# Performance work log

Hardware: AMD Instinct MI355X
Metric: run time of the kernel (lower is better)

Reference implementation:

```python
import jax, jax.numpy as jnp
import numpy as np


def _lstm_bi(x, wih, whh, b):
    # x: [B,T,D]; wih: [2,D,4H]; whh: [2,H,4H]; b: [2,4H]. PyTorch gate order i,f,g,o.
    def run(xs, wi, wh, bb):
        B, H = xs.shape[1], wh.shape[0]
        def step(carry, xt):
            h, c = carry
            g = xt @ wi + h @ wh + bb
            i, f, gg, o = jnp.split(g, 4, axis=-1)
            c = jax.nn.sigmoid(f) * c + jax.nn.sigmoid(i) * jnp.tanh(gg)
            h = jax.nn.sigmoid(o) * jnp.tanh(c)
            return (h, c), h
        z0 = jnp.zeros((B, H), xs.dtype)
        _, hs = jax.lax.scan(step, (z0, z0), xs)
        return hs
    xs = jnp.swapaxes(x, 0, 1)  # [T,B,D]
    hf = run(xs, wih[0], whh[0], b[0])
    hb = run(xs[::-1], wih[1], whh[1], b[1])[::-1]
    return jnp.swapaxes(jnp.concatenate([hf, hb], axis=-1), 0, 1)


def _norm_thr(att, thr):
    # sum-normalize, threshold-sparsify, renormalize (PSP core)
    att = att / (jnp.sum(att, -1, keepdims=True) + 1e-8)
    att = jnp.where(att > thr, att, jnp.zeros_like(att))
    return att / (jnp.sum(att, -1, keepdims=True) + 1e-8)


def _ln(x, g, b):
    mu = jnp.mean(x, -1, keepdims=True)
    var = jnp.mean(jnp.square(x - mu), -1, keepdims=True)
    return (x - mu) / jnp.sqrt(var + 1e-6) * g + b


def _forward(audio, video, thr_val, fa_w1, fa_w2, av_aw, av_ab, av_vw, av_vb,
             av_v2w, av_gw, av_hw, fv_w1, fv_w2, la_wih, la_whh, la_b,
             lv_wih, lv_whh, lv_b, vL1, vL2, aL1, aL2, vfc, afc, ln_g, ln_b, L1w, L2w):
    bs, T = audio.shape[0], audio.shape[1]
    fa = (audio @ fa_w1) @ fa_w2                          # [B,T,128]
    vf = video.reshape(bs, T, -1, video.shape[-1])        # [B,T,49,512]
    # AVGA audio-guided visual attention
    v_h = jax.nn.relu(vf @ av_vw + av_vb)                 # [B,T,49,512]
    a_h = jax.nn.relu(fa @ av_aw + av_ab)                 # [B,T,512]
    content = v_h @ av_v2w + (a_h @ av_gw)[..., None]     # [B,T,49,49]
    z = jnp.squeeze(jnp.tanh(content) @ av_hw, -1)        # [B,T,49]
    alpha = jax.nn.softmax(z, -1)
    video_t = jnp.einsum('btp,btpd->btd', alpha, vf)      # [B,T,512]
    video_t = (video_t @ fv_w1) @ fv_w2                   # [B,T,128]
    # bidirectional LSTMs
    lstm_a = _lstm_bi(fa, la_wih, la_whh, la_b)           # [B,T,256]
    lstm_v = _lstm_bi(video_t, lv_wih, lv_whh, lv_b)      # [B,T,256]
    # PSP (eval mode: dropout is identity)
    v_b1 = jax.nn.relu(lstm_v @ vL1)
    v_b2 = jax.nn.relu(lstm_v @ vL2)
    a_b1 = jax.nn.relu(lstm_a @ aL1)
    a_b2 = jax.nn.relu(lstm_a @ aL2)
    scale = 1.0 / jnp.sqrt(jnp.asarray(v_b2.shape[-1], v_b2.dtype))
    att = jax.nn.relu(jnp.einsum('bvd,bad->bva', v_b2, a_b1) * scale)  # v->a raw
    att_v2a = _norm_thr(att, thr_val)
    att_a2v = _norm_thr(jnp.swapaxes(att, 1, 2), thr_val)
    v_psp = lstm_v + jnp.einsum('bva,bad->bvd', att_v2a, a_b2)
    a_psp = lstm_a + jnp.einsum('bav,bvd->bad', att_a2v, v_b1)
    v_psp = _ln(jax.nn.relu(v_psp @ vfc), ln_g, ln_b)
    a_psp = _ln(jax.nn.relu(a_psp @ afc), ln_g, ln_b)
    fuse = 0.5 * (v_psp + a_psp)
    vn = v_psp / jnp.maximum(jnp.linalg.norm(v_psp, axis=-1, keepdims=True), 1e-12)
    an = a_psp / jnp.maximum(jnp.linalg.norm(a_psp, axis=-1, keepdims=True), 1e-12)
    cross_att = jnp.sum(vn * an, -1)                      # [B,T]
    out = jax.nn.relu(fuse @ L1w) @ L2w                   # [B,T,29]
    return (fuse, out, cross_att)


def setup_inputs() -> dict:
    key = jax.random.key(0)
    ks = iter(jax.random.split(key, 40))
    def w(*shape):
        fan_in = shape[-2] if len(shape) > 1 else shape[-1]
        return jax.random.normal(next(ks), shape, jnp.float32) * (1.0 / np.sqrt(fan_in))
    B, T = 256, 10
    return dict(
        audio=jax.random.normal(next(ks), (B, T, 128), jnp.float32),
        video=jax.random.normal(next(ks), (B, T, 7, 7, 512), jnp.float32),
        thr_val=jnp.float32(0.099),
        fa_w1=w(128, 256), fa_w2=w(256, 128),
        av_aw=w(128, 512), av_ab=jnp.zeros((512,), jnp.float32),
        av_vw=w(512, 512), av_vb=jnp.zeros((512,), jnp.float32),
        av_v2w=w(512, 49), av_gw=w(512, 49), av_hw=w(49, 1),
        fv_w1=w(512, 256), fv_w2=w(256, 128),
        la_wih=w(2, 128, 512), la_whh=w(2, 128, 512), la_b=jnp.zeros((2, 512), jnp.float32),
        lv_wih=w(2, 128, 512), lv_whh=w(2, 128, 512), lv_b=jnp.zeros((2, 512), jnp.float32),
        vL1=w(256, 256), vL2=w(256, 256), aL1=w(256, 256), aL2=w(256, 256),
        vfc=w(256, 256), afc=w(256, 256),
        ln_g=jnp.ones((256,), jnp.float32), ln_b=jnp.zeros((256,), jnp.float32),
        L1w=w(256, 64), L2w=w(64, 29),
    )


def reference(audio, video, thr_val, fa_w1, fa_w2, av_aw, av_ab, av_vw, av_vb,
              av_v2w, av_gw, av_hw, fv_w1, fv_w2, la_wih, la_whh, la_b,
              lv_wih, lv_whh, lv_b, vL1, vL2, aL1, aL2, vfc, afc, ln_g, ln_b, L1w, L2w):
    return _forward(audio, video, thr_val, fa_w1, fa_w2, av_aw, av_ab, av_vw, av_vb,
                    av_v2w, av_gw, av_hw, fv_w1, fv_w2, la_wih, la_whh, la_b,
                    lv_wih, lv_whh, lv_b, vL1, vL2, aL1, aL2, vfc, afc, ln_g, ln_b, L1w, L2w)
```

## Files before the change

### kernel.cpp

```cpp
#include <hip/hip_runtime.h>
#include <math.h>

#define DEV __device__ __forceinline__

typedef _Float16 f16x8 __attribute__((ext_vector_type(8)));
typedef _Float16 f16x4 __attribute__((ext_vector_type(4)));
typedef float    f32x4 __attribute__((ext_vector_type(4)));

typedef __attribute__((address_space(1))) const void gvoid_t;
typedef __attribute__((address_space(3))) void lvoid_t;

DEV void gload_lds16(const char* g, char* l){
    __builtin_amdgcn_global_load_lds((gvoid_t*)g, (lvoid_t*)l, 16, 0, 0);
}

DEV float sigmoidf_(float x){ return 1.0f/(1.0f + expf(-x)); }

DEV float wred64(float x){
    #pragma unroll
    for (int off=32; off; off>>=1) x += __shfl_xor(x, off);
    return x;
}

#define MFMA16(a,b,c) __builtin_amdgcn_mfma_f32_16x16x32_f16(a,b,c,0,0,0)

DEV void packone(const float* __restrict__ src, int N, int NfrTot, int nfOff,
                 _Float16* __restrict__ Dh, _Float16* __restrict__ Dl, int o){
    int j = o&7, l16 = (o>>3)&15, kg = (o>>7)&3;
    int rest = o>>9;
    int nfl = rest % (N>>4), kt = rest / (N>>4);
    int k = kt*32 + kg*8 + j, n = nfl*16 + l16;
    float x = src[(size_t)k*N + n];
    _Float16 h = (_Float16)x;
    size_t d = ((size_t)kt*NfrTot + nfOff + nfl)*512 + kg*128 + l16*8 + j;
    Dh[d] = h; Dl[d] = (_Float16)(x - (float)h);
}

__global__ __launch_bounds__(256) void k_prep(
    const float* __restrict__ fa_w1, const float* __restrict__ fa_w2, float* __restrict__ faW,
    const float* __restrict__ fv_w1, const float* __restrict__ fv_w2,
    const float* __restrict__ av_vw, _Float16* __restrict__ Bh, _Float16* __restrict__ Bl,
    const float* __restrict__ v2w, _Float16* __restrict__ Wh, _Float16* __restrict__ Wl,
    const float* __restrict__ lv_wih,
    _Float16* __restrict__ PKfv_h, _Float16* __restrict__ PKfv_l,
    _Float16* __restrict__ PKxv_h, _Float16* __restrict__ PKxv_l)
{
    int bid = blockIdx.x, t = threadIdx.x;
    if (bid < 64){
        int idx = bid*256+t; int m = idx>>7, n = idx&127;
        float acc=0.f;
        for (int k=0;k<256;k++) acc += fa_w1[m*256+k]*fa_w2[k*128+n];
        faW[idx]=acc;
    } else if (bid < 1088){
        int o = (bid-64)*256+t;
        int j = o & 7, l16 = (o>>3)&15, kg = (o>>7)&3, nf = (o>>9)&31, kt = o>>14;
        int k = kt*32 + kg*8 + j, n = nf*16 + l16;
        float x = av_vw[(size_t)k*512 + n];
        _Float16 h = (_Float16)x;
        Bh[o] = h; Bl[o] = (_Float16)(x - (float)h);
    } else if (bid < 1216){
        int o = (bid-1088)*256+t;
        int j = o & 7, l16 = (o>>3)&15, kg = (o>>7)&3, qf = (o>>9)&3, kbg = o>>11;
        int k = kbg*32 + kg*8 + j, q = qf*16 + l16;
        float x = (q < 49) ? v2w[(size_t)k*49 + q] : 0.f;
        _Float16 h = (_Float16)x;
        Wh[o] = h; Wl[o] = (_Float16)(x - (float)h);
    } else if (bid < 1472){
        int o = (bid-1216)*256+t;
        int j=o&7, l16=(o>>3)&15, kg=(o>>7)&3; int rest=o>>9;
        int nfl = rest&7, kt = rest>>3;
        int k = kt*32+kg*8+j, n = nfl*16+l16;
        float acc=0.f;
        for (int kk=0;kk<256;kk++) acc += fv_w1[k*256+kk]*fv_w2[kk*128+n];
        _Float16 h=(_Float16)acc;
        size_t d = ((size_t)kt*8 + nfl)*512 + kg*128 + l16*8 + j;
        PKfv_h[d]=h; PKfv_l[d]=(_Float16)(acc-(float)h);
    } else {
        int seg = (bid-1472)>>8;
        int o = ((bid-1472)&255)*256+t;
        packone(lv_wih + (size_t)seg*65536, 512, 64, seg*32, PKxv_h, PKxv_l, o);
    }
}

__global__ __launch_bounds__(256) void k_faga2(
    const float* __restrict__ audio, const float* __restrict__ faW,
    const float* __restrict__ av_aw, const float* __restrict__ av_ab,
    const float* __restrict__ av_gw,
    const float* __restrict__ la_wih, const float* __restrict__ la_b,
    float* __restrict__ gGA, float* __restrict__ xpA)
{
    int b0 = blockIdx.x*8; int t = threadIdx.x;
    __shared__ float sau[8][128], sfa[8][128], sah[8][512];
    for (int i=t;i<1024;i+=256){ int bt=i>>7,k=i&127; sau[bt][k]=audio[(size_t)(b0+bt)*128+k]; }
    __syncthreads();
    for (int u=0;u<4;u++){
        int i=t+u*256, bt=i>>7, n=i&127;
        float acc=0.f;
        for (int k4=0;k4<32;k4++){
            float4 x4=*(const float4*)&sau[bt][k4*4];
            acc+=x4.x*faW[(k4*4)*128+n]+x4.y*faW[(k4*4+1)*128+n]
                +x4.z*faW[(k4*4+2)*128+n]+x4.w*faW[(k4*4+3)*128+n];
        }
        sfa[bt][n]=acc;
    }
    __syncthreads();
    for (int u=0;u<2;u++){
        int n=t+u*256;
        float bv=av_ab[n];
        float acc[8]={bv,bv,bv,bv,bv,bv,bv,bv};
        for (int k4=0;k4<32;k4++){
            float w0=av_aw[(k4*4)*512+n], w1=av_aw[(k4*4+1)*512+n],
                  w2=av_aw[(k4*4+2)*512+n], w3=av_aw[(k4*4+3)*512+n];
            #pragma unroll
            for (int bt=0;bt<8;bt++){
                float4 x4=*(const float4*)&sfa[bt][k4*4];
                acc[bt]+=x4.x*w0+x4.y*w1+x4.z*w2+x4.w*w3;
            }
        }
        #pragma unroll
        for (int bt=0;bt<8;bt++) sah[bt][n]=fmaxf(acc[bt],0.f);
    }
    __syncthreads();
    for (int hh=0;hh<2;hh++){
        if (t<196){
            int bt=hh*4 + t/49, q=t%49;
            float acc=0.f;
            for (int k=0;k<512;k++) acc+=sah[bt][k]*av_gw[k*49+q];
            gGA[(size_t)(b0+bt)*49+q]=acc;
        }
    }
    for (int u=0;u<4;u++){
        int n = t + u*256;
        int dir = n >> 9, g = n & 511;
        const float* W = la_wih + (size_t)dir*65536;
        float bvv = la_b[dir*512 + g];
        float acc[8] = {bvv,bvv,bvv,bvv,bvv,bvv,bvv,bvv};
        for (int k4=0;k4<32;k4++){
            float w0=W[(k4*4+0)*512+g], w1=W[(k4*4+1)*512+g],
                  w2=W[(k4*4+2)*512+g], w3=W[(k4*4+3)*512+g];
            #pragma unroll
            for (int bt=0;bt<8;bt++){
                float4 x4=*(const float4*)&sfa[bt][k4*4];
                acc[bt]+=x4.x*w0+x4.y*w1+x4.z*w2+x4.w*w3;
            }
        }
        #pragma unroll
        for (int bt=0;bt<8;bt++)
            xpA[((size_t)(b0+bt))*1024 + n] = acc[bt];
    }
}

DEV void cvt4_(float4 v, f16x4& hv, f16x4& lv){
    hv[0]=(_Float16)v.x; lv[0]=(_Float16)(v.x-(float)hv[0]);
    hv[1]=(_Float16)v.y; lv[1]=(_Float16)(v.y-(float)hv[1]);
    hv[2]=(_Float16)v.z; lv[2]=(_Float16)(v.z-(float)hv[2]);
    hv[3]=(_Float16)v.w; lv[3]=(_Float16)(v.w-(float)hv[3]);
}

__global__ __launch_bounds__(256,2) void k_avga_fused(
    const float* __restrict__ video,
    const _Float16* __restrict__ Bh, const _Float16* __restrict__ Bl,
    const float* __restrict__ bias,
    const _Float16* __restrict__ Wh, const _Float16* __restrict__ Wl,
    const float* __restrict__ gGA, const float* __restrict__ hw,
    float* __restrict__ vT)
{
    __shared__ __align__(16) char smem[81920];
    int bt = blockIdx.x;
    int t = threadIdx.x;
    int lane = t & 63, w = t >> 6;
    int l16 = lane & 15, lq = lane >> 4;
    int lb = lane * 16;
    int w8 = w*8192;
    const char* BhB = (const char*)Bh;

    int am = t >> 3, ak = (t & 7) * 4;
    int aoff1 = ((am>>4)*4 + (ak>>3))*256 + (am&15)*16 + (ak&7)*2;
    int am2 = am + 32;
    int aoff2 = ((am2>>4)*4 + (ak>>3))*256 + (am2&15)*16 + (ak&7)*2;
    size_t r1 = (size_t)bt*49 + am;  if (r1 > 125439) r1 = 125439;
    size_t r2 = (size_t)bt*49 + am2; if (r2 > 125439) r2 = 125439;
    const float* Arow1 = video + r1*512 + ak;
    const float* Arow2 = video + r2*512 + ak;

    const f32x4 vzero = {0.f,0.f,0.f,0.f};
    f32x4 acc[4][8];
    #pragma unroll
    for (int p=0;p<4;p++)
        #pragma unroll
        for (int q=0;q<8;q++) acc[p][q] = vzero;

    float4 pa0, pa1;
    pa0 = *(const float4*)(Arow1);
    pa1 = *(const float4*)(Arow2);
    {
        f16x4 hv, lv;
        char* h = &smem[0];
        cvt4_(pa0, hv, lv);
        *(f16x4*)(h + aoff1) = hv; *(f16x4*)(h + 4096 + aoff1) = lv;
        cvt4_(pa1, hv, lv);
        *(f16x4*)(h + aoff2) = hv; *(f16x4*)(h + 4096 + aoff2) = lv;
        #pragma unroll
        for (int i=0;i<8;i++)
            gload_lds16(BhB + w8 + i*1024 + lane*16,
                        &smem[16384] + w8 + i*1024 + lane*16);
    }
    __syncthreads();

    for (int kt = 0; kt < 16; ++kt){
        int cur = kt & 1;
        bool more = (kt < 15);
        if (more){
            pa0 = *(const float4*)(Arow1 + (kt+1)*32);
            pa1 = *(const float4*)(Arow2 + (kt+1)*32);
            const char* srcb = BhB + (size_t)(kt+1)*32768 + w8;
            char* dstb = &smem[16384 + (cur^1)*32768] + w8;
            #pragma unroll
            for (int i=0;i<8;i++)
                gload_lds16(srcb + i*1024 + lane*16, dstb + i*1024 + lane*16);
        }
        const char* aB = &smem[cur*8192];
        f16x8 ah[4], al[4];
        #pragma unroll
        for (int p=0;p<4;p++){
            ah[p] = *(const f16x8*)(aB + p*1024 + lb);
            al[p] = *(const f16x8*)(aB + 4096 + p*1024 + lb);
        }
        const char* bB = &smem[16384 + cur*32768];
        #pragma unroll
        for (int q=0;q<8;q++){
            f16x8 bh  = *(const f16x8*)(bB + (w*8+q)*1024 + lb);
            f16x8 bl2 = *(const f16x8*)(Bl + (size_t)kt*16384 + (size_t)(w*8+q)*512 + lane*8);
            #pragma unroll
            for (int p=0;p<4;p++){
                acc[p][q] = MFMA16(ah[p], bh,  acc[p][q]);
                acc[p][q] = MFMA16(ah[p], bl2, acc[p][q]);
                acc[p][q] = MFMA16(al[p], bh,  acc[p][q]);
            }
        }
        if (more){
            char* h = &smem[(cur^1)*8192];
            f16x4 hv, lv;
            cvt4_(pa0, hv, lv);
            *(f16x4*)(h + aoff1) = hv; *(f16x4*)(h + 4096 + aoff1) = lv;
            cvt4_(pa1, hv, lv);
            *(f16x4*)(h + aoff2) = hv; *(f16x4*)(h + 4096 + aoff2) = lv;
        }
        __syncthreads();
    }

    float bv[8];
    #pragma unroll
    for (int q=0;q<8;q++) bv[q] = bias[w*128 + q*16 + l16];

    char* vh = &smem[16384 + w*8192];
    f32x4 cacc[4][4];
    #pragma unroll
    for (int p=0;p<4;p++)
        #pragma unroll
        for (int qf=0;qf<4;qf++) cacc[p][qf] = vzero;

    #pragma unroll
    for (int c=0;c<4;c++){
        #pragma unroll
        for (int p=0;p<4;p++)
            #pragma unroll
            for (int qq=0;qq<2;qq++){
                int q = c*2 + qq;
                int offbase = p*1024 + (qq*2 + (l16>>3))*256 + (l16&7)*2;
                #pragma unroll
                for (int r=0;r<4;r++){
                    float x = fmaxf(acc[p][q][r] + bv[q], 0.f);
                    _Float16 hh = (_Float16)x;
                    _Float16 ll = (_Float16)(x - (float)hh);
                    int off = offbase + (lq*4 + r)*16;
                    *(_Float16*)(vh + off)        = hh;
                    *(_Float16*)(vh + 4096 + off) = ll;
                }
            }
        int kbg = w*4 + c;
        f16x8 vhh[4], vhl[4];
        #pragma unroll
        for (int p=0;p<4;p++){
            vhh[p] = *(const f16x8*)(vh + p*1024 + lb);
            vhl[p] = *(const f16x8*)(vh + 4096 + p*1024 + lb);
        }
        #pragma unroll
        for (int qf=0;qf<4;qf++){
            size_t wo = (size_t)kbg*2048 + qf*512 + lane*8;
            f16x8 wh = *(const f16x8*)(Wh + wo);
            f16x8 wl = *(const f16x8*)(Wl + wo);
            #pragma unroll
            for (int p=0;p<4;p++){
                cacc[p][qf] = MFMA16(vhh[p], wh, cacc[p][qf]);
                cacc[p][qf] = MFMA16(vhh[p], wl, cacc[p][qf]);
                cacc[p][qf] = MFMA16(vhl[p], wh, cacc[p][qf]);
            }
        }
    }

    __syncthreads();
    float* pw = (float*)&smem[w*16384];
    #pragma unroll
    for (int p=0;p<4;p++)
        #pragma unroll
        for (int qf=0;qf<4;qf++)
            #pragma unroll
            for (int r=0;r<4;r++)
                pw[(p*16 + lq*4 + r)*64 + qf*16 + l16] = cacc[p][qf][r];
    __syncthreads();
    float* cb = (float*)&smem[0];
    for (int i=t; i<4096; i+=256)
        cb[i] = cb[i] + cb[4096+i] + cb[8192+i] + cb[12288+i];
    __syncthreads();

    float* szp    = (float*)&smem[65536];
    float* salpha = (float*)&smem[66560];
    if (t < 196){
        int p = t >> 2, ds = t & 3;
        float ga = gGA[(size_t)bt*49 + p];
        float part = 0.f;
        for (int q = ds*13; q < ds*13+13 && q < 49; q++)
            part += tanhf(cb[p*64 + q] + ga) * hw[q];
        szp[t] = part;
    }
    __syncthreads();
    if (t < 64){
        float z = (t<49) ? (szp[t*4]+szp[t*4+1]+szp[t*4+2]+szp[t*4+3]) : -1e30f;
        float m = z;
        #pragma unroll
        for (int off=32; off; off>>=1) m = fmaxf(m, __shfl_xor(m, off));
        float e = (t<49)? expf(z - m) : 0.f;
        float s = e;
        #pragma unroll
        for (int off=32; off; off>>=1) s += __shfl_xor(s, off);
        salpha[t] = e / s;
    }
    __syncthreads();
    const float* vb = video + (size_t)bt*49*512;
    #pragma unroll
    for (int u=0;u<2;u++){
        int d = t + u*256;
        float a0 = 0.f;
        for (int p=0;p<49;p++) a0 += salpha[p] * vb[(size_t)p*512 + d];
        vT[(size_t)bt*512 + d] = a0;
    }
}

template<int MP, int NQ, bool BIAS, bool RELU>
__global__ __launch_bounds__(256) void k_gemm(
    const float* __restrict__ A, int lda,
    const _Float16* __restrict__ Wh, const _Float16* __restrict__ Wl,
    const float* __restrict__ bias,
    float* __restrict__ C, int ldc,
    int nkt, int Nfr)
{
    __shared__ __align__(16) char sA[2][MP*2048];
    int t = threadIdx.x, lane = t&63, w = t>>6;
    int l16 = lane&15, lq = lane>>4, lb = lane*16;
    int row0 = blockIdx.x * (MP*16);
    int nf0 = blockIdx.y * (4*NQ) + w*NQ;

    int am = t>>3, ak = (t&7)*4;
    int aoff = ((am>>4)*4 + (ak>>3))*256 + (am&15)*16 + (ak&7)*2;
    const float* Arow = A + (size_t)(row0+am)*lda + ak;

    const f32x4 vzero = {0.f,0.f,0.f,0.f};
    f32x4 acc[MP][NQ];
    #pragma unroll
    for (int p=0;p<MP;p++)
        #pragma unroll
        for (int q=0;q<NQ;q++) acc[p][q] = vzero;

    float4 pa = *(const float4*)(Arow);
    {
        f16x4 hv, lv;
        char* h = &sA[0][0];
        cvt4_(pa, hv, lv);
        *(f16x4*)(h + aoff) = hv; *(f16x4*)(h + MP*1024 + aoff) = lv;
    }
    __syncthreads();

    for (int kt = 0; kt < nkt; ++kt){
        int cur = kt & 1;
        bool more = (kt+1 < nkt);
        if (more) pa = *(const float4*)(Arow + (kt+1)*32);
        const char* aB = &sA[cur][0];
        f16x8 ah[MP], al[MP];
        #pragma unroll
        for (int p=0;p<MP;p++){
            ah[p] = *(const f16x8*)(aB + p*1024 + lb);
            al[p] = *(const f16x8*)(aB + MP*1024 + p*1024 + lb);
        }
        #pragma unroll
        for (int q=0;q<NQ;q++){
            size_t bo = ((size_t)kt*Nfr + nf0 + q)*512 + lane*8;
            f16x8 bh  = *(const f16x8*)(Wh + bo);
            f16x8 bl2 = *(const f16x8*)(Wl + bo);
            #pragma unroll
            for (int p=0;p<MP;p++){
                acc[p][q] = MFMA16(ah[p], bh,  acc[p][q]);
                acc[p][q] = MFMA16(ah[p], bl2, acc[p][q]);
                acc[p][q] = MFMA16(al[p], bh,  acc[p][q]);
            }
        }
        if (more){
            char* h = &sA[cur^1][0];
            f16x4 hv, lv;
            cvt4_(pa, hv, lv);
            *(f16x4*)(h + aoff) = hv; *(f16x4*)(h + MP*1024 + aoff) = lv;
        }
        __syncthreads();
    }

    #pragma unroll
    for (int q=0;q<NQ;q++){
        int n = (nf0+q)*16 + l16;
        float bv = BIAS ? bias[n] : 0.f;
        #pragma unroll
        for (int p=0;p<MP;p++){
            #pragma unroll
            for (int r=0;r<4;r++){
                float v = acc[p][q][r] + bv;
                if (RELU) v = fmaxf(v, 0.f);
                C[(size_t)(row0 + p*16 + lq*4 + r)*ldc + n] = v;
            }
        }
    }
}

__global__ __launch_bounds__(256) void k_lstm(
    const float* __restrict__ xpA, const float* __restrict__ xpV,
    const float* __restrict__ la_whh, const float* __restrict__ lv_whh,
    float* __restrict__ lstm_a, float* __restrict__ lstm_v)
{
    int blk = blockIdx.x;
    int c = blk >> 6;
    int chunk = blk & 63;
    int t = threadIdx.x;
    int j  = t & 127;
    int bh = t >> 7;
    const float* whh = ((c<2)? la_whh : lv_whh) + (size_t)(c&1)*128*512;
    const float* xpm = (c<2)? xpA : xpV;
    float* outp = (c<2)? lstm_a : lstm_v;
    int dir = c & 1;

    __shared__ float hbuf[4][128];
    float cc[2] = {0.f,0.f};
    for (int i=t;i<512;i+=256) ((float*)hbuf)[i] = 0.f;
    __syncthreads();

    for (int s=0; s<10; s++){
        int tt = dir ? (9-s) : s;
        float gi[2], gf[2], gg[2], go[2];
        #pragma unroll
        for (int b=0;b<2;b++){
            int gb = chunk*4 + bh*2 + b;
            const float* xrow = xpm + ((size_t)gb*10 + tt)*1024 + dir*512;
            gi[b]=xrow[j]; gf[b]=xrow[128+j]; gg[b]=xrow[256+j]; go[b]=xrow[384+j];
        }
        #pragma unroll 4
        for (int k=0;k<128;k++){
            float wi = whh[k*512 + j];
            float wf = whh[k*512 + 128 + j];
            float wg = whh[k*512 + 256 + j];
            float wo = whh[k*512 + 384 + j];
            #pragma unroll
            for (int b=0;b<2;b++){
                float hk = hbuf[bh*2+b][k];
                gi[b] += hk*wi; gf[b] += hk*wf; gg[b] += hk*wg; go[b] += hk*wo;
            }
        }
        __syncthreads();
        #pragma unroll
        for (int b=0;b<2;b++){
            float i_ = sigmoidf_(gi[b]);
            float f_ = sigmoidf_(gf[b]);
            float g_ = tanhf(gg[b]);
            float o_ = sigmoidf_(go[b]);
            cc[b] = f_*cc[b] + i_*g_;
            float h_ = o_*tanhf(cc[b]);
            hbuf[bh*2+b][j] = h_;
            int gb = chunk*4 + bh*2 + b;
            outp[((size_t)gb*10 + tt)*256 + dir*128 + j] = h_;
        }
        __syncthreads();
    }
}

__global__ __launch_bounds__(256) void k_tail(
    const float* __restrict__ lstm_a, const float* __restrict__ lstm_v,
    const float* __restrict__ vL1, const float* __restrict__ vL2,
    const float* __restrict__ aL1, const float* __restrict__ aL2,
    const float* __restrict__ vfc, const float* __restrict__ afc,
    const float* __restrict__ thrp,
    const float* __restrict__ ln_g, const float* __restrict__ ln_b,
    const float* __restrict__ L1w, const float* __restrict__ L2w,
    float* __restrict__ dout)
{
    int b = blockIdx.x, t = threadIdx.x;
    int lane = t & 63, w = t >> 6;
    __shared__ float sla[10][256], slv[10][256];
    __shared__ float sb1v[10][256], sb2v[10][256], sb1a[10][256], sb2a[10][256];
    __shared__ float sfu[10][256];
    __shared__ float s64[10][64];
    __shared__ float satt[100], s_v2a[100], s_a2v[100];
    __shared__ float sredp[160];
    __shared__ float scos[120];

    size_t base = (size_t)b*2560;
    for (int i=t;i<2560;i+=256){
        ((float*)sla)[i] = lstm_a[base+i];
        ((float*)slv)[i] = lstm_v[base+i];
    }
    __syncthreads();

    {
        float a1[10], a2[10];
        #pragma unroll
        for (int r=0;r<10;r++){ a1[r]=0.f; a2[r]=0.f; }
        #pragma unroll 4
        for (int k=0;k<256;k++){
            float w1 = vL1[k*256+t], w2 = vL2[k*256+t];
            #pragma unroll
            for (int r=0;r<10;r++){ float x=slv[r][k]; a1[r]+=x*w1; a2[r]+=x*w2; }
        }
        #pragma unroll
        for (int r=0;r<10;r++){ sb1v[r][t]=fmaxf(a1[r],0.f); sb2v[r][t]=fmaxf(a2[r],0.f); }
        #pragma unroll
        for (int r=0;r<10;r++){ a1[r]=0.f; a2[r]=0.f; }
        #pragma unroll 4
        for (int k=0;k<256;k++){
            float w1 = aL1[k*256+t], w2 = aL2[k*256+t];
            #pragma unroll
            for (int r=0;r<10;r++){ float x=sla[r][k]; a1[r]+=x*w1; a2[r]+=x*w2; }
        }
        #pragma unroll
        for (int r=0;r<10;r++){ sb1a[r][t]=fmaxf(a1[r],0.f); sb2a[r][t]=fmaxf(a2[r],0.f); }
    }
    __syncthreads();

    if (t < 100){
        int v = t/10, a = t - v*10;
        float acc=0.f;
        for (int k=0;k<256;k++) acc += sb2v[v][k]*sb1a[a][k];
        satt[t] = fmaxf(acc*(1.0f/16.0f), 0.f);
    }
    __syncthreads();
    float thr = thrp[0];
    if (t < 10){
        int v = t;
        float rs=0.f; for(int a=0;a<10;a++) rs += satt[v*10+a];
        float inv = 1.f/(rs+1e-8f);
        float tmp[10]; float rs2=0.f;
        for(int a=0;a<10;a++){ float x = satt[v*10+a]*inv; x = (x>thr)?x:0.f; tmp[a]=x; rs2+=x; }
        float inv2 = 1.f/(rs2+1e-8f);
        for(int a=0;a<10;a++) s_v2a[v*10+a] = tmp[a]*inv2;
    } else if (t>=16 && t<26){
        int a = t-16;
        float cs=0.f; for(int v=0;v<10;v++) cs += satt[v*10+a];
        float inv = 1.f/(cs+1e-8f);
        float tmp[10]; float cs2=0.f;
        for(int v=0;v<10;v++){ float x = satt[v*10+a]*inv; x=(x>thr)?x:0.f; tmp[v]=x; cs2+=x; }
        float inv2 = 1.f/(cs2+1e-8f);
        for(int v=0;v<10;v++) s_a2v[a*10+v] = tmp[v]*inv2;
    }
    __syncthreads();

    #pragma unroll
    for (int v=0;v<10;v++){
        float acc = slv[v][t];
        #pragma unroll
        for (int a=0;a<10;a++) acc += s_v2a[v*10+a]*sb2a[a][t];
        slv[v][t] = acc;
    }
    #pragma unroll
    for (int a=0;a<10;a++){
        float acc = sla[a][t];
        #pragma unroll
        for (int v=0;v<10;v++) acc += s_a2v[a*10+v]*sb1v[v][t];
        sla[a][t] = acc;
    }
    __syncthreads();

    float fv[10], fa2[10];
    #pragma unroll
    for (int r=0;r<10;r++){ fv[r]=0.f; fa2[r]=0.f; }
    #pragma unroll 4
    for (int k=0;k<256;k++){
        float wv = vfc[k*256+t], wa = afc[k*256+t];
        #pragma unroll
        for (int r=0;r<10;r++){ fv[r]+=slv[r][k]*wv; fa2[r]+=sla[r][k]*wa; }
    }
    #pragma unroll
    for (int r=0;r<10;r++){ fv[r]=fmaxf(fv[r],0.f); fa2[r]=fmaxf(fa2[r],0.f); }

    #pragma unroll
    for (int r=0;r<10;r++){
        float s1 = wred64(fv[r]);
        float s2 = wred64(fv[r]*fv[r]);
        float s3 = wred64(fa2[r]);
        float s4 = wred64(fa2[r]*fa2[r]);
        if (lane==0){
            sredp[r*16 + 0*4 + w] = s1; sredp[r*16 + 1*4 + w] = s2;
            sredp[r*16 + 2*4 + w] = s3; sredp[r*16 + 3*4 + w] = s4;
        }
    }
    __syncthreads();
    float gt = ln_g[t], bt2 = ln_b[t];
    #pragma unroll
    for (int r=0;r<10;r++){
        float s1 = sredp[r*16+0]+sredp[r*16+1]+sredp[r*16+2]+sredp[r*16+3];
        float s2 = sredp[r*16+4]+sredp[r*16+5]+sredp[r*16+6]+sredp[r*16+7];
        float s3 = sredp[r*16+8]+sredp[r*16+9]+sredp[r*16+10]+sredp[r*16+11];
        float s4 = sredp[r*16+12]+sredp[r*16+13]+sredp[r*16+14]+sredp[r*16+15];
        float muv = s1*(1.f/256.f);
        float varv = s2*(1.f/256.f) - muv*muv;
        float rsv = 1.f/sqrtf(varv+1e-6f);
        float vln = (fv[r]-muv)*rsv*gt + bt2;
        float mua = s3*(1.f/256.f);
        float vara = s4*(1.f/256.f) - mua*mua;
        float rsa = 1.f/sqrtf(vara+1e-6f);
        float aln = (fa2[r]-mua)*rsa*gt + bt2;
        float fu = 0.5f*(vln+aln);
        dout[(size_t)(b*10+r)*256 + t] = fu;
        sfu[r][t] = fu;
        float c1 = wred64(vln*vln);
        float c2 = wred64(aln*aln);
        float c3 = wred64(vln*aln);
        if (lane==0){
            scos[r*12 + 0*4 + w] = c1; scos[r*12 + 1*4 + w] = c2; scos[r*12 + 2*4 + w] = c3;
        }
    }
    __syncthreads();
    if (t < 10){
        int r = t;
        float nv2 = scos[r*12+0]+scos[r*12+1]+scos[r*12+2]+scos[r*12+3];
        float na2 = scos[r*12+4]+scos[r*12+5]+scos[r*12+6]+scos[r*12+7];
        float dva = scos[r*12+8]+scos[r*12+9]+scos[r*12+10]+scos[r*12+11];
        float nv = fmaxf(sqrtf(nv2), 1e-12f);
        float na = fmaxf(sqrtf(na2), 1e-12f);
        dout[729600 + b*10 + r] = dva/(nv*na);
    }

    #pragma unroll
    for (int pass=0; pass<3; ++pass){
        int r = pass*4 + w;
        if (r < 10){
            float acc = 0.f;
            for (int k4=0;k4<64;k4++){
                float4 f4 = *(const float4*)&sfu[r][k4*4];
                acc += f4.x*L1w[(k4*4)*64+lane] + f4.y*L1w[(k4*4+1)*64+lane]
                     + f4.z*L1w[(k4*4+2)*64+lane] + f4.w*L1w[(k4*4+3)*64+lane];
            }
            s64[r][lane] = fmaxf(acc, 0.f);
        }
    }
    __syncthreads();
    for (int i=t; i<290; i+=256){
        int r = i/29, jj = i - r*29;
        float acc = 0.f;
        #pragma unroll
        for (int k=0;k<64;k++) acc += s64[r][k]*L2w[k*29+jj];
        dout[655360 + (size_t)(b*10+r)*29 + jj] = acc;
    }
}

extern "C" void kernel_launch(void* const* d_in, const int* in_sizes, int n_in,
                              void* d_out, int out_size, void* d_ws, size_t ws_size,
                              hipStream_t stream) {
    const float* audio  = (const float*)d_in[0];
    const float* video  = (const float*)d_in[1];
    const float* thrp   = (const float*)d_in[2];
    const float* fa_w1  = (const float*)d_in[3];
    const float* fa_w2  = (const float*)d_in[4];
    const float* av_aw  = (const float*)d_in[5];
    const float* av_ab  = (const float*)d_in[6];
    const float* av_vw  = (const float*)d_in[7];
    const float* av_vb  = (const float*)d_in[8];
    const float* av_v2w = (const float*)d_in[9];
    const float* av_gw  = (const float*)d_in[10];
    const float* av_hw  = (const float*)d_in[11];
    const float* fv_w1  = (const float*)d_in[12];
    const float* fv_w2  = (const float*)d_in[13];
    const float* la_wih = (const float*)d_in[14];
    const float* la_whh = (const float*)d_in[15];
    const float* la_b   = (const float*)d_in[16];
    const float* lv_wih = (const float*)d_in[17];
    const float* lv_whh = (const float*)d_in[18];
    const float* lv_b   = (const float*)d_in[19];
    const float* vL1    = (const float*)d_in[20];
    const float* vL2    = (const float*)d_in[21];
    const float* aL1    = (const float*)d_in[22];
    const float* aL2    = (const float*)d_in[23];
    const float* vfc    = (const float*)d_in[24];
    const float* afc    = (const float*)d_in[25];
    const float* ln_g   = (const float*)d_in[26];
    const float* ln_b   = (const float*)d_in[27];
    const float* L1w    = (const float*)d_in[28];
    const float* L2w    = (const float*)d_in[29];
    float* dout = (float*)d_out;
    float* ws = (float*)d_ws;

    float* faW  = ws;
    float* gGA  = ws + 409600;
    float* vT   = ws + 535040;
    float* xpA  = ws + 2173440;
    float* xpV  = ws + 4794880;
    float* la   = ws + 7416320;
    float* lv   = ws + 8071680;
    _Float16* Bh = (_Float16*)(ws + 12659200);
    _Float16* Bl = (_Float16*)(ws + 12790272);
    _Float16* Wh = (_Float16*)(ws + 12921344);
    _Float16* Wl = (_Float16*)(ws + 12937728);
    _Float16* PKfv_h = (_Float16*)(ws + 12954112);
    _Float16* PKfv_l = (_Float16*)(ws + 12986880);
    _Float16* PKxv_h = (_Float16*)(ws + 13150720);
    _Float16* PKxv_l = (_Float16*)(ws + 13216256);
    float* vfea = ws + 13675008;

    k_prep<<<1984, 256, 0, stream>>>(fa_w1, fa_w2, faW, fv_w1, fv_w2,
                                     av_vw, Bh, Bl, av_v2w, Wh, Wl,
                                     lv_wih, PKfv_h, PKfv_l, PKxv_h, PKxv_l);
    k_faga2<<<320, 256, 0, stream>>>(audio, faW, av_aw, av_ab, av_gw,
                                     la_wih, la_b, gGA, xpA);
    k_avga_fused<<<2560, 256, 0, stream>>>(video, Bh, Bl, av_vb, Wh, Wl,
                                           gGA, av_hw, vT);
    k_gemm<2,2,false,false><<<dim3(80,1), 256, 0, stream>>>(
        vT, 512, PKfv_h, PKfv_l, nullptr, vfea, 128, 16, 8);
    k_gemm<2,4,true,false><<<dim3(80,4), 256, 0, stream>>>(
        vfea, 128, PKxv_h, PKxv_l, lv_b, xpV, 1024, 4, 64);
    k_lstm<<<256, 256, 0, stream>>>(xpA, xpV, la_whh, lv_whh, la, lv);
    k_tail<<<256, 256, 0, stream>>>(la, lv, vL1, vL2, aL1, aL2, vfc, afc,
                                    thrp, ln_g, ln_b, L1w, L2w, dout);
}
```

Before: 675.0 us.

## Stream AVGA weights directly from global and fuse the two video GEMMs

The AVGA kernel stops staging the high-half weight tiles into LDS with async global-to-LDS loads. It now reads both weight halves straight from global/L2 and double-buffers only the converted activation tiles, two k-steps at a time. This cuts LDS use from 80KB to about 66KB, which may help occupancy, but it adds more global loads inside the MFMA loop. Separately, the fv projection GEMM and the xpV GEMM are merged into one kernel that keeps the 128-wide intermediate in shared memory. That drops one launch and the global round trip for it, at the cost of recomputing the first GEMM in each of the four column blocks.

```diff
diff --git a/kernel.cpp b/kernel.cpp
--- a/kernel.cpp
+++ b/kernel.cpp
@@ -6,13 +6,6 @@
 typedef _Float16 f16x8 __attribute__((ext_vector_type(8)));
 typedef _Float16 f16x4 __attribute__((ext_vector_type(4)));
 typedef float    f32x4 __attribute__((ext_vector_type(4)));
-
-typedef __attribute__((address_space(1))) const void gvoid_t;
-typedef __attribute__((address_space(3))) void lvoid_t;
-
-DEV void gload_lds16(const char* g, char* l){
-    __builtin_amdgcn_global_load_lds((gvoid_t*)g, (lvoid_t*)l, 16, 0, 0);
-}
 
 DEV float sigmoidf_(float x){ return 1.0f/(1.0f + expf(-x)); }
 
@@ -165,14 +158,12 @@
     const float* __restrict__ gGA, const float* __restrict__ hw,
     float* __restrict__ vT)
 {
-    __shared__ __align__(16) char smem[81920];
+    __shared__ __align__(16) char smem[67072];
     int bt = blockIdx.x;
     int t = threadIdx.x;
     int lane = t & 63, w = t >> 6;
     int l16 = lane & 15, lq = lane >> 4;
     int lb = lane * 16;
-    int w8 = w*8192;
-    const char* BhB = (const char*)Bh;
 
     int am = t >> 3, ak = (t & 7) * 4;
     int aoff1 = ((am>>4)*4 + (ak>>3))*256 + (am&15)*16 + (ak&7)*2;
@@ -190,61 +181,71 @@
         #pragma unroll
         for (int q=0;q<8;q++) acc[p][q] = vzero;
 
-    float4 pa0, pa1;
-    pa0 = *(const float4*)(Arow1);
-    pa1 = *(const float4*)(Arow2);
+    float4 paA0, paA1, paB0, paB1;
+    paA0 = *(const float4*)(Arow1);
+    paA1 = *(const float4*)(Arow2);
+    paB0 = *(const float4*)(Arow1 + 32);
+    paB1 = *(const float4*)(Arow2 + 32);
     {
         f16x4 hv, lv;
-        char* h = &smem[0];
-        cvt4_(pa0, hv, lv);
-        *(f16x4*)(h + aoff1) = hv; *(f16x4*)(h + 4096 + aoff1) = lv;
-        cvt4_(pa1, hv, lv);
-        *(f16x4*)(h + aoff2) = hv; *(f16x4*)(h + 4096 + aoff2) = lv;
-        #pragma unroll
-        for (int i=0;i<8;i++)
-            gload_lds16(BhB + w8 + i*1024 + lane*16,
-                        &smem[16384] + w8 + i*1024 + lane*16);
-    }
-    __syncthreads();
-
-    for (int kt = 0; kt < 16; ++kt){
-        int cur = kt & 1;
-        bool more = (kt < 15);
+        char* h0 = &smem[0];
+        cvt4_(paA0, hv, lv);
+        *(f16x4*)(h0 + aoff1) = hv; *(f16x4*)(h0 + 4096 + aoff1) = lv;
+        cvt4_(paA1, hv, lv);
+        *(f16x4*)(h0 + aoff2) = hv; *(f16x4*)(h0 + 4096 + aoff2) = lv;
+        char* h1 = &smem[8192];
+        cvt4_(paB0, hv, lv);
+        *(f16x4*)(h1 + aoff1) = hv; *(f16x4*)(h1 + 4096 + aoff1) = lv;
+        cvt4_(paB1, hv, lv);
+        *(f16x4*)(h1 + aoff2) = hv; *(f16x4*)(h1 + 4096 + aoff2) = lv;
+    }
+    __syncthreads();
+
+    for (int skt = 0; skt < 8; ++skt){
+        int cur2 = (skt & 1) * 2;
+        bool more = (skt < 7);
         if (more){
-            pa0 = *(const float4*)(Arow1 + (kt+1)*32);
-            pa1 = *(const float4*)(Arow2 + (kt+1)*32);
-            const char* srcb = BhB + (size_t)(kt+1)*32768 + w8;
-            char* dstb = &smem[16384 + (cur^1)*32768] + w8;
-            #pragma unroll
-            for (int i=0;i<8;i++)
-                gload_lds16(srcb + i*1024 + lane*16, dstb + i*1024 + lane*16);
-        }
-        const char* aB = &smem[cur*8192];
-        f16x8 ah[4], al[4];
-        #pragma unroll
-        for (int p=0;p<4;p++){
-            ah[p] = *(const f16x8*)(aB + p*1024 + lb);
-            al[p] = *(const f16x8*)(aB + 4096 + p*1024 + lb);
-        }
-        const char* bB = &smem[16384 + cur*32768];
-        #pragma unroll
-        for (int q=0;q<8;q++){
-            f16x8 bh  = *(const f16x8*)(bB + (w*8+q)*1024 + lb);
-            f16x8 bl2 = *(const f16x8*)(Bl + (size_t)kt*16384 + (size_t)(w*8+q)*512 + lane*8);
+            int ko = (skt+1)*64;
+            paA0 = *(const float4*)(Arow1 + ko);
+            paA1 = *(const float4*)(Arow2 + ko);
+            paB0 = *(const float4*)(Arow1 + ko + 32);
+            paB1 = *(const float4*)(Arow2 + ko + 32);
+        }
+        #pragma unroll
+        for (int kk=0; kk<2; ++kk){
+            int kt = skt*2 + kk;
+            const char* aB = &smem[(cur2+kk)*8192];
+            f16x8 ah[4], al[4];
             #pragma unroll
             for (int p=0;p<4;p++){
-                acc[p][q] = MFMA16(ah[p], bh,  acc[p][q]);
-                acc[p][q] = MFMA16(ah[p], bl2, acc[p][q]);
-                acc[p][q] = MFMA16(al[p], bh,  acc[p][q]);
+                ah[p] = *(const f16x8*)(aB + p*1024 + lb);
+                al[p] = *(const f16x8*)(aB + 4096 + p*1024 + lb);
+            }
+            #pragma unroll
+            for (int q=0;q<8;q++){
+                size_t bo = (size_t)kt*16384 + (size_t)(w*8 + q)*512 + lane*8;
+                f16x8 bh  = *(const f16x8*)(Bh + bo);
+                f16x8 bl2 = *(const f16x8*)(Bl + bo);
+                #pragma unroll
+                for (int p=0;p<4;p++){
+                    acc[p][q] = MFMA16(ah[p], bh,  acc[p][q]);
+                    acc[p][q] = MFMA16(ah[p], bl2, acc[p][q]);
+                    acc[p][q] = MFMA16(al[p], bh,  acc[p][q]);
+                }
             }
         }
         if (more){
-            char* h = &smem[(cur^1)*8192];
             f16x4 hv, lv;
-            cvt4_(pa0, hv, lv);
-            *(f16x4*)(h + aoff1) = hv; *(f16x4*)(h + 4096 + aoff1) = lv;
-            cvt4_(pa1, hv, lv);
-            *(f16x4*)(h + aoff2) = hv; *(f16x4*)(h + 4096 + aoff2) = lv;
+            char* h0 = &smem[(cur2^2)*8192];
+            cvt4_(paA0, hv, lv);
+            *(f16x4*)(h0 + aoff1) = hv; *(f16x4*)(h0 + 4096 + aoff1) = lv;
+            cvt4_(paA1, hv, lv);
+            *(f16x4*)(h0 + aoff2) = hv; *(f16x4*)(h0 + 4096 + aoff2) = lv;
+            char* h1 = &smem[((cur2^2)+1)*8192];
+            cvt4_(paB0, hv, lv);
+            *(f16x4*)(h1 + aoff1) = hv; *(f16x4*)(h1 + 4096 + aoff1) = lv;
+            cvt4_(paB1, hv, lv);
+            *(f16x4*)(h1 + aoff2) = hv; *(f16x4*)(h1 + 4096 + aoff2) = lv;
         }
         __syncthreads();
     }
@@ -253,7 +254,7 @@
     #pragma unroll
     for (int q=0;q<8;q++) bv[q] = bias[w*128 + q*16 + l16];
 
-    char* vh = &smem[16384 + w*8192];
+    char* vh = &smem[w*8192];
     f32x4 cacc[4][4];
     #pragma unroll
     for (int p=0;p<4;p++)
@@ -347,84 +348,135 @@
     }
 }
 
-template<int MP, int NQ, bool BIAS, bool RELU>
-__global__ __launch_bounds__(256) void k_gemm(
-    const float* __restrict__ A, int lda,
-    const _Float16* __restrict__ Wh, const _Float16* __restrict__ Wl,
-    const float* __restrict__ bias,
-    float* __restrict__ C, int ldc,
-    int nkt, int Nfr)
+__global__ __launch_bounds__(256) void k_gemm2(
+    const float* __restrict__ vT,
+    const _Float16* __restrict__ Fh, const _Float16* __restrict__ Fl,
+    const _Float16* __restrict__ Xh, const _Float16* __restrict__ Xl,
+    const float* __restrict__ lv_b,
+    float* __restrict__ xpV)
 {
-    __shared__ __align__(16) char sA[2][MP*2048];
+    __shared__ __align__(16) char sA[2][4096];
+    __shared__ float sV[32][132];
     int t = threadIdx.x, lane = t&63, w = t>>6;
     int l16 = lane&15, lq = lane>>4, lb = lane*16;
-    int row0 = blockIdx.x * (MP*16);
-    int nf0 = blockIdx.y * (4*NQ) + w*NQ;
+    int row0 = blockIdx.x * 32;
 
     int am = t>>3, ak = (t&7)*4;
     int aoff = ((am>>4)*4 + (ak>>3))*256 + (am&15)*16 + (ak&7)*2;
-    const float* Arow = A + (size_t)(row0+am)*lda + ak;
+    const float* Arow = vT + (size_t)(row0+am)*512 + ak;
 
     const f32x4 vzero = {0.f,0.f,0.f,0.f};
-    f32x4 acc[MP][NQ];
-    #pragma unroll
-    for (int p=0;p<MP;p++)
-        #pragma unroll
-        for (int q=0;q<NQ;q++) acc[p][q] = vzero;
+    f32x4 acc1[2][2];
+    #pragma unroll
+    for (int p=0;p<2;p++)
+        #pragma unroll
+        for (int q=0;q<2;q++) acc1[p][q] = vzero;
 
     float4 pa = *(const float4*)(Arow);
     {
         f16x4 hv, lv;
         char* h = &sA[0][0];
         cvt4_(pa, hv, lv);
-        *(f16x4*)(h + aoff) = hv; *(f16x4*)(h + MP*1024 + aoff) = lv;
-    }
-    __syncthreads();
-
-    for (int kt = 0; kt < nkt; ++kt){
+        *(f16x4*)(h + aoff) = hv; *(f16x4*)(h + 2048 + aoff) = lv;
+    }
+    __syncthreads();
+    for (int kt = 0; kt < 16; ++kt){
         int cur = kt & 1;
-        bool more = (kt+1 < nkt);
+        bool more = (kt < 15);
         if (more) pa = *(const float4*)(Arow + (kt+1)*32);
         const char* aB = &sA[cur][0];
-        f16x8 ah[MP], al[MP];
-        #pragma unroll
-        for (int p=0;p<MP;p++){
+        f16x8 ah[2], al[2];
+        #pragma unroll
+        for (int p=0;p<2;p++){
             ah[p] = *(const f16x8*)(aB + p*1024 + lb);
-            al[p] = *(const f16x8*)(aB + MP*1024 + p*1024 + lb);
-        }
-        #pragma unroll
-        for (int q=0;q<NQ;q++){
-            size_t bo = ((size_t)kt*Nfr + nf0 + q)*512 + lane*8;
-            f16x8 bh  = *(const f16x8*)(Wh + bo);
-            f16x8 bl2 = *(const f16x8*)(Wl + bo);
-            #pragma unroll
-            for (int p=0;p<MP;p++){
-                acc[p][q] = MFMA16(ah[p], bh,  acc[p][q]);
-                acc[p][q] = MFMA16(ah[p], bl2, acc[p][q]);
-                acc[p][q] = MFMA16(al[p], bh,  acc[p][q]);
+            al[p] = *(const f16x8*)(aB + 2048 + p*1024 + lb);
+        }
+        #pragma unroll
+        for (int q=0;q<2;q++){
+            size_t bo = ((size_t)kt*8 + w*2 + q)*512 + lane*8;
+            f16x8 bh  = *(const f16x8*)(Fh + bo);
+            f16x8 bl2 = *(const f16x8*)(Fl + bo);
+            #pragma unroll
+            for (int p=0;p<2;p++){
+                acc1[p][q] = MFMA16(ah[p], bh,  acc1[p][q]);
+                acc1[p][q] = MFMA16(ah[p], bl2, acc1[p][q]);
+                acc1[p][q] = MFMA16(al[p], bh,  acc1[p][q]);
             }
         }
         if (more){
             char* h = &sA[cur^1][0];
             f16x4 hv, lv;
             cvt4_(pa, hv, lv);
-            *(f16x4*)(h + aoff) = hv; *(f16x4*)(h + MP*1024 + aoff) = lv;
+            *(f16x4*)(h + aoff) = hv; *(f16x4*)(h + 2048 + aoff) = lv;
         }
         __syncthreads();
     }
-
-    #pragma unroll
-    for (int q=0;q<NQ;q++){
+    #pragma unroll
+    for (int q=0;q<2;q++){
+        int n = (w*2+q)*16 + l16;
+        #pragma unroll
+        for (int p=0;p<2;p++)
+            #pragma unroll
+            for (int r=0;r<4;r++)
+                sV[p*16 + lq*4 + r][n] = acc1[p][q][r];
+    }
+    __syncthreads();
+
+    int nf0 = blockIdx.y*16 + w*4;
+    f32x4 acc2[2][4];
+    #pragma unroll
+    for (int p=0;p<2;p++)
+        #pragma unroll
+        for (int q=0;q<4;q++) acc2[p][q] = vzero;
+
+    pa = *(const float4*)&sV[am][ak];
+    {
+        f16x4 hv, lv;
+        char* h = &sA[0][0];
+        cvt4_(pa, hv, lv);
+        *(f16x4*)(h + aoff) = hv; *(f16x4*)(h + 2048 + aoff) = lv;
+    }
+    __syncthreads();
+    for (int kt = 0; kt < 4; ++kt){
+        int cur = kt & 1;
+        bool more = (kt < 3);
+        if (more) pa = *(const float4*)&sV[am][(kt+1)*32 + ak];
+        const char* aB = &sA[cur][0];
+        f16x8 ah[2], al[2];
+        #pragma unroll
+        for (int p=0;p<2;p++){
+            ah[p] = *(const f16x8*)(aB + p*1024 + lb);
+            al[p] = *(const f16x8*)(aB + 2048 + p*1024 + lb);
+        }
+        #pragma unroll
+        for (int q=0;q<4;q++){
+            size_t bo = ((size_t)kt*64 + nf0 + q)*512 + lane*8;
+            f16x8 bh  = *(const f16x8*)(Xh + bo);
+            f16x8 bl2 = *(const f16x8*)(Xl + bo);
+            #pragma unroll
+            for (int p=0;p<2;p++){
+                acc2[p][q] = MFMA16(ah[p], bh,  acc2[p][q]);
+                acc2[p][q] = MFMA16(ah[p], bl2, acc2[p][q]);
+                acc2[p][q] = MFMA16(al[p], bh,  acc2[p][q]);
+            }
+        }
+        if (more){
+            char* h = &sA[cur^1][0];
+            f16x4 hv, lv;
+            cvt4_(pa, hv, lv);
+            *(f16x4*)(h + aoff) = hv; *(f16x4*)(h + 2048 + aoff) = lv;
+        }
+        __syncthreads();
+    }
+    #pragma unroll
+    for (int q=0;q<4;q++){
         int n = (nf0+q)*16 + l16;
-        float bv = BIAS ? bias[n] : 0.f;
-        #pragma unroll
-        for (int p=0;p<MP;p++){
-            #pragma unroll
-            for (int r=0;r<4;r++){
-                float v = acc[p][q][r] + bv;
-                if (RELU) v = fmaxf(v, 0.f);
-                C[(size_t)(row0 + p*16 + lq*4 + r)*ldc + n] = v;
-            }
+        float bv = lv_b[n];
+        #pragma unroll
+        for (int p=0;p<2;p++){
+            #pragma unroll
+            for (int r=0;r<4;r++)
+                xpV[(size_t)(row0 + p*16 + lq*4 + r)*1024 + n] = acc2[p][q][r] + bv;
         }
     }
 }
@@ -717,7 +769,6 @@
     _Float16* PKfv_l = (_Float16*)(ws + 12986880);
     _Float16* PKxv_h = (_Float16*)(ws + 13150720);
     _Float16* PKxv_l = (_Float16*)(ws + 13216256);
-    float* vfea = ws + 13675008;
 
     k_prep<<<1984, 256, 0, stream>>>(fa_w1, fa_w2, faW, fv_w1, fv_w2,
                                      av_vw, Bh, Bl, av_v2w, Wh, Wl,
@@ -726,10 +777,8 @@
                                      la_wih, la_b, gGA, xpA);
     k_avga_fused<<<2560, 256, 0, stream>>>(video, Bh, Bl, av_vb, Wh, Wl,
                                            gGA, av_hw, vT);
-    k_gemm<2,2,false,false><<<dim3(80,1), 256, 0, stream>>>(
-        vT, 512, PKfv_h, PKfv_l, nullptr, vfea, 128, 16, 8);
-    k_gemm<2,4,true,false><<<dim3(80,4), 256, 0, stream>>>(
-        vfea, 128, PKxv_h, PKxv_l, lv_b, xpV, 1024, 4, 64);
+    k_gemm2<<<dim3(80,4), 256, 0, stream>>>(vT, PKfv_h, PKfv_l,
+                                            PKxv_h, PKxv_l, lv_b, xpV);
     k_lstm<<<256, 256, 0, stream>>>(xpA, xpV, la_whh, lv_whh, la, lv);
     k_tail<<<256, 256, 0, stream>>>(la, lv, vL1, vL2, aL1, aL2, vfc, afc,
                                     thrp, ln_g, ln_b, L1w, L2w, dout);
```

New measurement: 668.5 us. Within noise of the previous version (-1.0%).
